# Kernel tuning notes

Hardware: AMD Instinct MI355X
Metric: run time of the kernel (lower is better)

The kernel has to match this reference:

```python
import jax, jax.numpy as jnp
import numpy as np

N = 50000      # nodes
E = 800000     # edges (avg degree 16)
IN, H, OUT = 512, 128, 64
L = 4          # num GCN layers
ALPHA = 0.1


def setup_inputs() -> dict:
    key = jax.random.key(0)
    ks = jax.random.split(key, 9)
    # GPRGNN layer weights: temp[k] = alpha*(1-alpha)^k, temp[L] = (1-alpha)^L
    temp = ALPHA * (1.0 - ALPHA) ** np.arange(L + 1)
    temp[-1] = (1.0 - ALPHA) ** L
    return {
        "x": jax.random.normal(ks[0], (N, IN), jnp.float32),
        "w": jax.random.uniform(ks[1], (E,), jnp.float32),
        "W_in": jax.random.normal(ks[2], (IN, H), jnp.float32) * (1.0 / np.sqrt(IN)),
        "b_in": jnp.zeros((H,), jnp.float32),
        "Wl": jax.random.normal(ks[3], (L, H, H), jnp.float32) * (1.0 / np.sqrt(H)),
        "bl": jnp.zeros((L, H), jnp.float32),
        "temp": jnp.asarray(temp, jnp.float32),
        "W_out": jax.random.normal(ks[4], (H, OUT), jnp.float32) * (1.0 / np.sqrt(H)),
        "b_out": jnp.zeros((OUT,), jnp.float32),
        "src": jax.random.randint(ks[5], (E,), 0, N, jnp.int32),
        "dst": jax.random.randint(ks[6], (E,), 0, N, jnp.int32),
    }


def reference(x, w, W_in, b_in, Wl, bl, temp, W_out, b_out, src, dst):
    # input linear projection
    h = x @ W_in + b_in                         # [N, H]
    hidden = temp[0] * h
    xcur = h
    for i in range(L):
        m = xcur @ Wl[i] + bl[i]                # per-layer GCN linear, [N, H]
        msg = w[:, None] * m[src]               # weighted gather, [E, H]
        agg = jax.ops.segment_sum(msg, dst, num_segments=N)  # scatter-sum, [N, H]
        xcur = jax.nn.relu(agg)                 # (dropout is eval-mode no-op)
        hidden = hidden + temp[i + 1] * xcur
    return hidden @ W_out + b_out               # [N, OUT]
```

## Files before the change

kernel.cpp:

```cpp
#include <hip/hip_runtime.h>


typedef __attribute__((ext_vector_type(8))) short short8;
typedef __attribute__((ext_vector_type(4))) float f32x4;

__device__ __forceinline__ unsigned short f2bf(float f) {
  union { float f; unsigned u; } c{f};
  unsigned u = c.u;
  return (unsigned short)((u + 0x7fff + ((u >> 16) & 1)) >> 16);
}
__device__ __forceinline__ float bf2f_lo(unsigned v) {
  return __uint_as_float(v << 16);
}
__device__ __forceinline__ float bf2f_hi(unsigned v) {
  return __uint_as_float(v & 0xffff0000u);
}
__device__ __forceinline__ unsigned pack2bf(float a, float b) {
  return (unsigned)f2bf(a) | ((unsigned)f2bf(b) << 16);
}

__device__ __forceinline__ void gll16(const void* g, void* l) {
  __builtin_amdgcn_global_load_lds(
      (const __attribute__((address_space(1))) unsigned int*)g,
      (__attribute__((address_space(3))) unsigned int*)l, 16, 0, 0);
}

__global__ void hist_kernel(const int* __restrict__ dst, int* __restrict__ deg, int E) {
  int e = blockIdx.x * blockDim.x + threadIdx.x;
  if (e < E) atomicAdd(&deg[dst[e]], 1);
}

__global__ __launch_bounds__(256) void scan_partial(const int* __restrict__ deg,
                                                    int* __restrict__ bsum, int N) {
  int b = blockIdx.x, t = threadIdx.x;
  int lane = t & 63, wave = t >> 6;
  int i0 = b * 1024 + t * 4;
  int s = 0;
  if (i0 + 3 < N) {
    int4 v = *(const int4*)&deg[i0];
    s = v.x + v.y + v.z + v.w;
  } else {
    for (int k = 0; k < 4; ++k)
      if (i0 + k < N) s += deg[i0 + k];
  }
  for (int d = 32; d; d >>= 1) s += __shfl_down(s, d, 64);
  __shared__ int ws[4];
  if (lane == 0) ws[wave] = s;
  __syncthreads();
  if (t == 0) bsum[b] = ws[0] + ws[1] + ws[2] + ws[3];
}

__global__ void scan_base(const int* __restrict__ bsum, int* __restrict__ base, int nb) {
  int l = threadIdx.x;
  int v = (l < nb) ? bsum[l] : 0;
  int incl = v;
  for (int d = 1; d < 64; d <<= 1) {
    int t = __shfl_up(incl, d, 64);
    if (l >= d) incl += t;
  }
  if (l < nb) base[l] = incl - v;
}

__global__ __launch_bounds__(256) void scan_emit(const int* __restrict__ deg,
                                                 const int* __restrict__ base,
                                                 int* __restrict__ rowptr,
                                                 int* __restrict__ cursor, int N, int E) {
  int b = blockIdx.x, t = threadIdx.x;
  int lane = t & 63, wave = t >> 6;
  int i0 = b * 1024 + t * 4;
  int d0 = 0, d1 = 0, d2 = 0, d3 = 0;
  if (i0 + 3 < N) {
    int4 v = *(const int4*)&deg[i0];
    d0 = v.x; d1 = v.y; d2 = v.z; d3 = v.w;
  } else {
    if (i0 < N) d0 = deg[i0];
    if (i0 + 1 < N) d1 = deg[i0 + 1];
    if (i0 + 2 < N) d2 = deg[i0 + 2];
    if (i0 + 3 < N) d3 = deg[i0 + 3];
  }
  int s = d0 + d1 + d2 + d3;
  int incl = s;
  for (int d = 1; d < 64; d <<= 1) {
    int tv = __shfl_up(incl, d, 64);
    if (lane >= d) incl += tv;
  }
  __shared__ int ws[4];
  if (lane == 63) ws[wave] = incl;
  __syncthreads();
  int woff = 0;
  for (int wv = 0; wv < wave; ++wv) woff += ws[wv];
  int off = base[b] + woff + incl - s;
  if (i0 < N)     { rowptr[i0] = off;                cursor[i0] = off; }
  if (i0 + 1 < N) { int o = off + d0;                rowptr[i0+1] = o; cursor[i0+1] = o; }
  if (i0 + 2 < N) { int o = off + d0 + d1;           rowptr[i0+2] = o; cursor[i0+2] = o; }
  if (i0 + 3 < N) { int o = off + d0 + d1 + d2;      rowptr[i0+3] = o; cursor[i0+3] = o; }
  if (b == 0 && t == 0) rowptr[N] = E;
}

__global__ void fill_kernel(const int* __restrict__ src, const int* __restrict__ dst,
                            const float* __restrict__ w, int* __restrict__ cursor,
                            int* __restrict__ esrc, float* __restrict__ ew, int E) {
  int e = blockIdx.x * blockDim.x + threadIdx.x;
  if (e < E) {
    int d = dst[e];
    int p = atomicAdd(&cursor[d], 1);
    esrc[p] = src[e];
    ew[p] = w[e];
  }
}

__global__ void conv_w_kernel(const float* __restrict__ W_in,
                              const float* __restrict__ Wl,
                              const float* __restrict__ W_out,
                              unsigned short* __restrict__ WinT,
                              unsigned short* __restrict__ WlT,
                              unsigned short* __restrict__ WoutT) {
  int o = blockIdx.x * blockDim.x + threadIdx.x;
  if (o < 65536) {
    int n = o >> 9, k = o & 511;
    WinT[o] = f2bf(W_in[k * 128 + n]);
  } else if (o < 131072) {
    int p = o - 65536;
    int layer = p >> 14, n = (p >> 7) & 127, k = p & 127;
    WlT[p] = f2bf(Wl[layer * 16384 + k * 128 + n]);
  } else if (o < 139264) {
    int p = o - 131072;
    int n = p >> 7, k = p & 127;
    WoutT[p] = f2bf(W_out[k * 64 + n]);
  }
}

template <int K, bool CONV>
__global__ __launch_bounds__(256) void gemm_bf16(
    const void* __restrict__ Ain, const unsigned short* __restrict__ BT,
    const float* __restrict__ bias, unsigned short* __restrict__ Cb, int M) {
  __shared__ unsigned short As[128 * 32];
  __shared__ unsigned short Bs[128 * 32];

  const int tid = threadIdx.x;
  const int lane = tid & 63;
  const int wave = tid >> 6;
  const int wm = (wave & 1) * 64;
  const int wn = (wave >> 1) * 64;
  const int blockRow = blockIdx.x * 128;

  f32x4 acc[4][4];
#pragma unroll
  for (int i = 0; i < 4; ++i)
#pragma unroll
    for (int j = 0; j < 4; ++j) acc[i][j] = (f32x4){0.f, 0.f, 0.f, 0.f};

  for (int k0 = 0; k0 < K; k0 += 32) {
    __syncthreads();
    if (CONV) {
      const float* A = (const float*)Ain;
      int row = tid >> 1;
      int kc = (tid & 1) * 16;
      int grow = blockRow + row;
      if (grow >= M) grow = M - 1;
      const float* s = &A[(size_t)grow * K + k0 + kc];
      float4 v0 = *(const float4*)(s);
      float4 v1 = *(const float4*)(s + 4);
      float4 v2 = *(const float4*)(s + 8);
      float4 v3 = *(const float4*)(s + 12);
      uint4 p0, p1;
      p0.x = pack2bf(v0.x, v0.y); p0.y = pack2bf(v0.z, v0.w);
      p0.z = pack2bf(v1.x, v1.y); p0.w = pack2bf(v1.z, v1.w);
      p1.x = pack2bf(v2.x, v2.y); p1.y = pack2bf(v2.z, v2.w);
      p1.z = pack2bf(v3.x, v3.y); p1.w = pack2bf(v3.z, v3.w);
      *(uint4*)&As[row * 32 + kc] = p0;
      *(uint4*)&As[row * 32 + kc + 8] = p1;
    } else {
      const unsigned short* A = (const unsigned short*)Ain;
#pragma unroll
      for (int ch = wave; ch < 8; ch += 4) {
        int row = ch * 16 + (lane >> 2);
        int grow = blockRow + row;
        if (grow >= M) grow = M - 1;
        gll16(&A[(size_t)grow * K + k0 + (lane & 3) * 8], (char*)As + ch * 1024);
      }
    }
#pragma unroll
    for (int ch = wave; ch < 8; ch += 4) {
      int row = ch * 16 + (lane >> 2);
      gll16(&BT[(size_t)row * K + k0 + (lane & 3) * 8], (char*)Bs + ch * 1024);
    }
    __syncthreads();

    short8 af[4], bfr[4];
#pragma unroll
    for (int i = 0; i < 4; ++i)
      af[i] = *(const short8*)&As[(wm + i * 16 + (lane & 15)) * 32 + (lane >> 4) * 8];
#pragma unroll
    for (int j = 0; j < 4; ++j)
      bfr[j] = *(const short8*)&Bs[(wn + j * 16 + (lane & 15)) * 32 + (lane >> 4) * 8];
#pragma unroll
    for (int i = 0; i < 4; ++i)
#pragma unroll
      for (int j = 0; j < 4; ++j)
        acc[i][j] =
            __builtin_amdgcn_mfma_f32_16x16x32_bf16(af[i], bfr[j], acc[i][j], 0, 0, 0);
  }

#pragma unroll
  for (int j = 0; j < 4; ++j) {
    int col = wn + j * 16 + (lane & 15);
    float bj = bias[col];
#pragma unroll
    for (int i = 0; i < 4; ++i) {
#pragma unroll
      for (int r = 0; r < 4; ++r) {
        int row = blockRow + wm + i * 16 + (lane >> 4) * 4 + r;
        if (row < M) Cb[(size_t)row * 128 + col] = f2bf(acc[i][j][r] + bj);
      }
    }
  }
}

__global__ __launch_bounds__(256) void agg_v3(
    const int* __restrict__ rowptr, const int* __restrict__ esrc,
    const float* __restrict__ ew, const unsigned short* __restrict__ mb,
    unsigned short* __restrict__ xnext, int N) {
  const int node = blockIdx.x * 4 + (threadIdx.x >> 6);
  const int lane = threadIdx.x & 63;
  if (node >= N) return;
  const int g = lane >> 4;
  const int c = lane & 15;
  const int beg = rowptr[node];
  const int end = rowptr[node + 1];
  const unsigned short* mc = mb + c * 8;

  float aA[8] = {0.f, 0.f, 0.f, 0.f, 0.f, 0.f, 0.f, 0.f};
  float aB[8] = {0.f, 0.f, 0.f, 0.f, 0.f, 0.f, 0.f, 0.f};

  int j = beg;
  for (; j + 8 <= end; j += 8) {
    int sA = esrc[j + g];     float wA = ew[j + g];
    int sB = esrc[j + 4 + g]; float wB = ew[j + 4 + g];
    uint4 vA = *(const uint4*)&mc[(size_t)sA * 128];
    uint4 vB = *(const uint4*)&mc[(size_t)sB * 128];
    aA[0] = fmaf(wA, bf2f_lo(vA.x), aA[0]); aA[1] = fmaf(wA, bf2f_hi(vA.x), aA[1]);
    aA[2] = fmaf(wA, bf2f_lo(vA.y), aA[2]); aA[3] = fmaf(wA, bf2f_hi(vA.y), aA[3]);
    aA[4] = fmaf(wA, bf2f_lo(vA.z), aA[4]); aA[5] = fmaf(wA, bf2f_hi(vA.z), aA[5]);
    aA[6] = fmaf(wA, bf2f_lo(vA.w), aA[6]); aA[7] = fmaf(wA, bf2f_hi(vA.w), aA[7]);
    aB[0] = fmaf(wB, bf2f_lo(vB.x), aB[0]); aB[1] = fmaf(wB, bf2f_hi(vB.x), aB[1]);
    aB[2] = fmaf(wB, bf2f_lo(vB.y), aB[2]); aB[3] = fmaf(wB, bf2f_hi(vB.y), aB[3]);
    aB[4] = fmaf(wB, bf2f_lo(vB.z), aB[4]); aB[5] = fmaf(wB, bf2f_hi(vB.z), aB[5]);
    aB[6] = fmaf(wB, bf2f_lo(vB.w), aB[6]); aB[7] = fmaf(wB, bf2f_hi(vB.w), aB[7]);
  }
  if (j + 4 <= end) {
    int s = esrc[j + g]; float wt = ew[j + g];
    uint4 v = *(const uint4*)&mc[(size_t)s * 128];
    aA[0] = fmaf(wt, bf2f_lo(v.x), aA[0]); aA[1] = fmaf(wt, bf2f_hi(v.x), aA[1]);
    aA[2] = fmaf(wt, bf2f_lo(v.y), aA[2]); aA[3] = fmaf(wt, bf2f_hi(v.y), aA[3]);
    aA[4] = fmaf(wt, bf2f_lo(v.z), aA[4]); aA[5] = fmaf(wt, bf2f_hi(v.z), aA[5]);
    aA[6] = fmaf(wt, bf2f_lo(v.w), aA[6]); aA[7] = fmaf(wt, bf2f_hi(v.w), aA[7]);
    j += 4;
  }
  if (j < end) {
    int idx = j + g;
    int s = esrc[(idx < end) ? idx : (end - 1)];
    float wt = (idx < end) ? ew[idx] : 0.f;
    uint4 v = *(const uint4*)&mc[(size_t)s * 128];
    aB[0] = fmaf(wt, bf2f_lo(v.x), aB[0]); aB[1] = fmaf(wt, bf2f_hi(v.x), aB[1]);
    aB[2] = fmaf(wt, bf2f_lo(v.y), aB[2]); aB[3] = fmaf(wt, bf2f_hi(v.y), aB[3]);
    aB[4] = fmaf(wt, bf2f_lo(v.z), aB[4]); aB[5] = fmaf(wt, bf2f_hi(v.z), aB[5]);
    aB[6] = fmaf(wt, bf2f_lo(v.w), aB[6]); aB[7] = fmaf(wt, bf2f_hi(v.w), aB[7]);
  }

  float r[8];
#pragma unroll
  for (int k = 0; k < 8; ++k) {
    float s = aA[k] + aB[k];
    s += __shfl_xor(s, 16, 64);
    s += __shfl_xor(s, 32, 64);
    r[k] = fmaxf(s, 0.f);
  }
  if (g == 0) {
    uint4 pk;
    pk.x = pack2bf(r[0], r[1]);
    pk.y = pack2bf(r[2], r[3]);
    pk.z = pack2bf(r[4], r[5]);
    pk.w = pack2bf(r[6], r[7]);
    *(uint4*)&xnext[(size_t)node * 128 + c * 8] = pk;
  }
}

__global__ __launch_bounds__(256) void gemm_out(
    const unsigned short* __restrict__ xb,
    const float* __restrict__ temp, const unsigned short* __restrict__ WoT,
    const float* __restrict__ b_out, float* __restrict__ out, int M) {
  __shared__ unsigned short As[128 * 136];
  __shared__ unsigned short Bs[64 * 136];

  const int tid = threadIdx.x;
  const int lane = tid & 63;
  const int wave = tid >> 6;
  const int blockRow = blockIdx.x * 128;

  float t[5];
#pragma unroll
  for (int i = 0; i < 5; ++i) t[i] = temp[i];

  {
    int row = tid >> 1;
    int grow = blockRow + row;
    if (grow >= M) grow = M - 1;
    int ch0 = (tid & 1) * 64;
#pragma unroll
    for (int gch = 0; gch < 64; gch += 8) {
      float acc[8] = {0.f, 0.f, 0.f, 0.f, 0.f, 0.f, 0.f, 0.f};
#pragma unroll
      for (int i = 0; i < 5; ++i) {
        uint4 v = *(const uint4*)&xb[((size_t)i * M + grow) * 128 + ch0 + gch];
        acc[0] = fmaf(t[i], bf2f_lo(v.x), acc[0]);
        acc[1] = fmaf(t[i], bf2f_hi(v.x), acc[1]);
        acc[2] = fmaf(t[i], bf2f_lo(v.y), acc[2]);
        acc[3] = fmaf(t[i], bf2f_hi(v.y), acc[3]);
        acc[4] = fmaf(t[i], bf2f_lo(v.z), acc[4]);
        acc[5] = fmaf(t[i], bf2f_hi(v.z), acc[5]);
        acc[6] = fmaf(t[i], bf2f_lo(v.w), acc[6]);
        acc[7] = fmaf(t[i], bf2f_hi(v.w), acc[7]);
      }
      uint4 pk;
      pk.x = pack2bf(acc[0], acc[1]);
      pk.y = pack2bf(acc[2], acc[3]);
      pk.z = pack2bf(acc[4], acc[5]);
      pk.w = pack2bf(acc[6], acc[7]);
      *(uint4*)&As[row * 136 + ch0 + gch] = pk;
    }
  }
  for (int i = tid; i < 64 * 16; i += 256) {
    int row = i >> 4;
    int chunk = (i & 15) * 8;
    *(uint4*)&Bs[row * 136 + chunk] = *(const uint4*)&WoT[row * 128 + chunk];
  }
  __syncthreads();

  f32x4 acc[2][4];
#pragma unroll
  for (int i = 0; i < 2; ++i)
#pragma unroll
    for (int j = 0; j < 4; ++j) acc[i][j] = (f32x4){0.f, 0.f, 0.f, 0.f};

#pragma unroll
  for (int kf = 0; kf < 4; ++kf) {
    short8 af[2], bfr[4];
#pragma unroll
    for (int i = 0; i < 2; ++i)
      af[i] = *(const short8*)&As[(wave * 32 + i * 16 + (lane & 15)) * 136 + kf * 32 +
                                  (lane >> 4) * 8];
#pragma unroll
    for (int j = 0; j < 4; ++j)
      bfr[j] = *(const short8*)&Bs[(j * 16 + (lane & 15)) * 136 + kf * 32 +
                                   (lane >> 4) * 8];
#pragma unroll
    for (int i = 0; i < 2; ++i)
#pragma unroll
      for (int j = 0; j < 4; ++j)
        acc[i][j] =
            __builtin_amdgcn_mfma_f32_16x16x32_bf16(af[i], bfr[j], acc[i][j], 0, 0, 0);
  }

#pragma unroll
  for (int j = 0; j < 4; ++j) {
    int col = j * 16 + (lane & 15);
    float bj = b_out[col];
#pragma unroll
    for (int i = 0; i < 2; ++i) {
#pragma unroll
      for (int r = 0; r < 4; ++r) {
        int row = blockRow + wave * 32 + i * 16 + (lane >> 4) * 4 + r;
        if (row < M) out[(size_t)row * 64 + col] = acc[i][j][r] + bj;
      }
    }
  }
}

extern "C" void kernel_launch(void* const* d_in, const int* in_sizes, int n_in,
                              void* d_out, int out_size, void* d_ws, size_t ws_size,
                              hipStream_t stream) {
  const float* x     = (const float*)d_in[0];
  const float* w     = (const float*)d_in[1];
  const float* W_in  = (const float*)d_in[2];
  const float* b_in  = (const float*)d_in[3];
  const float* Wl    = (const float*)d_in[4];
  const float* bl    = (const float*)d_in[5];
  const float* temp  = (const float*)d_in[6];
  const float* W_out = (const float*)d_in[7];
  const float* b_out = (const float*)d_in[8];
  const int*   src   = (const int*)d_in[9];
  const int*   dst   = (const int*)d_in[10];

  const int IN = 512, H = 128, L = 4;
  const int N = in_sizes[0] / IN;
  const int E = in_sizes[1];
  const int NB = (N + 1023) / 1024;
  const size_t NH = (size_t)N * H;

  char* p = (char*)d_ws;
  auto alloc = [&](size_t bytes) {
    void* r = (void*)p;
    p += (bytes + 255) & ~(size_t)255;
    return r;
  };
  unsigned short* xb     = (unsigned short*)alloc(5 * NH * 2);
  unsigned short* mbuf_b = (unsigned short*)alloc(NH * 2);
  unsigned short* WinT   = (unsigned short*)alloc((size_t)H * IN * 2);
  unsigned short* WlT    = (unsigned short*)alloc((size_t)L * H * H * 2);
  unsigned short* WoutT  = (unsigned short*)alloc((size_t)64 * H * 2);
  int*   deg    = (int*)alloc((size_t)N * sizeof(int));
  int*   rowptr = (int*)alloc((size_t)(N + 1) * sizeof(int));
  int*   cursor = (int*)alloc((size_t)N * sizeof(int));
  int*   esrc   = (int*)alloc((size_t)E * sizeof(int));
  float* ew     = (float*)alloc((size_t)E * sizeof(float));
  int*   bsum   = (int*)alloc(64 * sizeof(int));
  int*   base   = (int*)alloc(64 * sizeof(int));

  hipMemsetAsync(deg, 0, (size_t)N * sizeof(int), stream);
  hist_kernel<<<(E + 255) / 256, 256, 0, stream>>>(dst, deg, E);
  scan_partial<<<NB, 256, 0, stream>>>(deg, bsum, N);
  scan_base<<<1, 64, 0, stream>>>(bsum, base, NB);
  scan_emit<<<NB, 256, 0, stream>>>(deg, base, rowptr, cursor, N, E);
  fill_kernel<<<(E + 255) / 256, 256, 0, stream>>>(src, dst, w, cursor, esrc, ew, E);
  conv_w_kernel<<<544, 256, 0, stream>>>(W_in, Wl, W_out, WinT, WlT, WoutT);

  const int gB = (N + 127) / 128;

  gemm_bf16<512, true><<<gB, 256, 0, stream>>>(x, WinT, b_in, xb, N);

  for (int i = 0; i < L; ++i) {
    gemm_bf16<128, false><<<gB, 256, 0, stream>>>(
        xb + (size_t)i * NH, WlT + (size_t)i * H * H, bl + (size_t)i * H, mbuf_b, N);
    agg_v3<<<(N + 3) / 4, 256, 0, stream>>>(rowptr, esrc, ew, mbuf_b,
                                            xb + (size_t)(i + 1) * NH, N);
  }

  gemm_out<<<gB, 256, 0, stream>>>(xb, temp, WoutT, b_out, (float*)d_out, N);
}
```

Before: 506.7 us.

## Aggregate before the linear transform and fuse gather with per-layer GEMM

Uses linearity to compute (A·x)·W + (Σw)·b in place of A·(x·W + b). Each block gathers neighbours for 128 nodes into LDS as bf16, then runs the 128x128 MFMA GEMM on that tile, adding the weight-sum-scaled bias and ReLU. This removes the intermediate message buffer round trip and one launch per layer. In exchange, the gather now runs with far fewer waves, each handling 32 nodes serially, so latency hiding drops. It also adds a bf16 rounding of the aggregate before the GEMM.

```diff
diff --git a/kernel.cpp b/kernel.cpp
--- a/kernel.cpp
+++ b/kernel.cpp
@@ -217,72 +217,142 @@
   }
 }
 
-__global__ __launch_bounds__(256) void agg_v3(
+__global__ __launch_bounds__(256) void layer_fused(
     const int* __restrict__ rowptr, const int* __restrict__ esrc,
-    const float* __restrict__ ew, const unsigned short* __restrict__ mb,
-    unsigned short* __restrict__ xnext, int N) {
-  const int node = blockIdx.x * 4 + (threadIdx.x >> 6);
-  const int lane = threadIdx.x & 63;
-  if (node >= N) return;
+    const float* __restrict__ ew, const unsigned short* __restrict__ xin,
+    const unsigned short* __restrict__ WlTl, const float* __restrict__ bl,
+    unsigned short* __restrict__ xout, int N) {
+  __shared__ unsigned short As[128 * 136];
+  __shared__ float wsumS[128];
+  __shared__ unsigned short Bs[128 * 32];
+
+  const int tid = threadIdx.x;
+  const int lane = tid & 63;
+  const int wave = tid >> 6;
   const int g = lane >> 4;
   const int c = lane & 15;
-  const int beg = rowptr[node];
-  const int end = rowptr[node + 1];
-  const unsigned short* mc = mb + c * 8;
-
-  float aA[8] = {0.f, 0.f, 0.f, 0.f, 0.f, 0.f, 0.f, 0.f};
-  float aB[8] = {0.f, 0.f, 0.f, 0.f, 0.f, 0.f, 0.f, 0.f};
-
-  int j = beg;
-  for (; j + 8 <= end; j += 8) {
-    int sA = esrc[j + g];     float wA = ew[j + g];
-    int sB = esrc[j + 4 + g]; float wB = ew[j + 4 + g];
-    uint4 vA = *(const uint4*)&mc[(size_t)sA * 128];
-    uint4 vB = *(const uint4*)&mc[(size_t)sB * 128];
-    aA[0] = fmaf(wA, bf2f_lo(vA.x), aA[0]); aA[1] = fmaf(wA, bf2f_hi(vA.x), aA[1]);
-    aA[2] = fmaf(wA, bf2f_lo(vA.y), aA[2]); aA[3] = fmaf(wA, bf2f_hi(vA.y), aA[3]);
-    aA[4] = fmaf(wA, bf2f_lo(vA.z), aA[4]); aA[5] = fmaf(wA, bf2f_hi(vA.z), aA[5]);
-    aA[6] = fmaf(wA, bf2f_lo(vA.w), aA[6]); aA[7] = fmaf(wA, bf2f_hi(vA.w), aA[7]);
-    aB[0] = fmaf(wB, bf2f_lo(vB.x), aB[0]); aB[1] = fmaf(wB, bf2f_hi(vB.x), aB[1]);
-    aB[2] = fmaf(wB, bf2f_lo(vB.y), aB[2]); aB[3] = fmaf(wB, bf2f_hi(vB.y), aB[3]);
-    aB[4] = fmaf(wB, bf2f_lo(vB.z), aB[4]); aB[5] = fmaf(wB, bf2f_hi(vB.z), aB[5]);
-    aB[6] = fmaf(wB, bf2f_lo(vB.w), aB[6]); aB[7] = fmaf(wB, bf2f_hi(vB.w), aB[7]);
-  }
-  if (j + 4 <= end) {
-    int s = esrc[j + g]; float wt = ew[j + g];
-    uint4 v = *(const uint4*)&mc[(size_t)s * 128];
-    aA[0] = fmaf(wt, bf2f_lo(v.x), aA[0]); aA[1] = fmaf(wt, bf2f_hi(v.x), aA[1]);
-    aA[2] = fmaf(wt, bf2f_lo(v.y), aA[2]); aA[3] = fmaf(wt, bf2f_hi(v.y), aA[3]);
-    aA[4] = fmaf(wt, bf2f_lo(v.z), aA[4]); aA[5] = fmaf(wt, bf2f_hi(v.z), aA[5]);
-    aA[6] = fmaf(wt, bf2f_lo(v.w), aA[6]); aA[7] = fmaf(wt, bf2f_hi(v.w), aA[7]);
-    j += 4;
-  }
-  if (j < end) {
-    int idx = j + g;
-    int s = esrc[(idx < end) ? idx : (end - 1)];
-    float wt = (idx < end) ? ew[idx] : 0.f;
-    uint4 v = *(const uint4*)&mc[(size_t)s * 128];
-    aB[0] = fmaf(wt, bf2f_lo(v.x), aB[0]); aB[1] = fmaf(wt, bf2f_hi(v.x), aB[1]);
-    aB[2] = fmaf(wt, bf2f_lo(v.y), aB[2]); aB[3] = fmaf(wt, bf2f_hi(v.y), aB[3]);
-    aB[4] = fmaf(wt, bf2f_lo(v.z), aB[4]); aB[5] = fmaf(wt, bf2f_hi(v.z), aB[5]);
-    aB[6] = fmaf(wt, bf2f_lo(v.w), aB[6]); aB[7] = fmaf(wt, bf2f_hi(v.w), aB[7]);
-  }
-
-  float r[8];
-#pragma unroll
-  for (int k = 0; k < 8; ++k) {
-    float s = aA[k] + aB[k];
-    s += __shfl_xor(s, 16, 64);
-    s += __shfl_xor(s, 32, 64);
-    r[k] = fmaxf(s, 0.f);
-  }
-  if (g == 0) {
-    uint4 pk;
-    pk.x = pack2bf(r[0], r[1]);
-    pk.y = pack2bf(r[2], r[3]);
-    pk.z = pack2bf(r[4], r[5]);
-    pk.w = pack2bf(r[6], r[7]);
-    *(uint4*)&xnext[(size_t)node * 128 + c * 8] = pk;
+  const int blockRow = blockIdx.x * 128;
+  const unsigned short* mc = xin + c * 8;
+
+  for (int t = 0; t < 32; ++t) {
+    const int nl = wave * 32 + t;
+    const int node = blockRow + nl;
+    float aA[8] = {0.f, 0.f, 0.f, 0.f, 0.f, 0.f, 0.f, 0.f};
+    float aB[8] = {0.f, 0.f, 0.f, 0.f, 0.f, 0.f, 0.f, 0.f};
+    float wsA = 0.f, wsB = 0.f;
+    if (node < N) {
+      const int beg = rowptr[node];
+      const int end = rowptr[node + 1];
+      int j = beg;
+      for (; j + 8 <= end; j += 8) {
+        int sA = esrc[j + g];     float wA = ew[j + g];
+        int sB = esrc[j + 4 + g]; float wB = ew[j + 4 + g];
+        uint4 vA = *(const uint4*)&mc[(size_t)sA * 128];
+        uint4 vB = *(const uint4*)&mc[(size_t)sB * 128];
+        wsA += wA; wsB += wB;
+        aA[0] = fmaf(wA, bf2f_lo(vA.x), aA[0]); aA[1] = fmaf(wA, bf2f_hi(vA.x), aA[1]);
+        aA[2] = fmaf(wA, bf2f_lo(vA.y), aA[2]); aA[3] = fmaf(wA, bf2f_hi(vA.y), aA[3]);
+        aA[4] = fmaf(wA, bf2f_lo(vA.z), aA[4]); aA[5] = fmaf(wA, bf2f_hi(vA.z), aA[5]);
+        aA[6] = fmaf(wA, bf2f_lo(vA.w), aA[6]); aA[7] = fmaf(wA, bf2f_hi(vA.w), aA[7]);
+        aB[0] = fmaf(wB, bf2f_lo(vB.x), aB[0]); aB[1] = fmaf(wB, bf2f_hi(vB.x), aB[1]);
+        aB[2] = fmaf(wB, bf2f_lo(vB.y), aB[2]); aB[3] = fmaf(wB, bf2f_hi(vB.y), aB[3]);
+        aB[4] = fmaf(wB, bf2f_lo(vB.z), aB[4]); aB[5] = fmaf(wB, bf2f_hi(vB.z), aB[5]);
+        aB[6] = fmaf(wB, bf2f_lo(vB.w), aB[6]); aB[7] = fmaf(wB, bf2f_hi(vB.w), aB[7]);
+      }
+      if (j + 4 <= end) {
+        int s = esrc[j + g]; float wt = ew[j + g];
+        uint4 v = *(const uint4*)&mc[(size_t)s * 128];
+        wsA += wt;
+        aA[0] = fmaf(wt, bf2f_lo(v.x), aA[0]); aA[1] = fmaf(wt, bf2f_hi(v.x), aA[1]);
+        aA[2] = fmaf(wt, bf2f_lo(v.y), aA[2]); aA[3] = fmaf(wt, bf2f_hi(v.y), aA[3]);
+        aA[4] = fmaf(wt, bf2f_lo(v.z), aA[4]); aA[5] = fmaf(wt, bf2f_hi(v.z), aA[5]);
+        aA[6] = fmaf(wt, bf2f_lo(v.w), aA[6]); aA[7] = fmaf(wt, bf2f_hi(v.w), aA[7]);
+        j += 4;
+      }
+      if (j < end) {
+        int idx = j + g;
+        int s = esrc[(idx < end) ? idx : (end - 1)];
+        float wt = (idx < end) ? ew[idx] : 0.f;
+        uint4 v = *(const uint4*)&mc[(size_t)s * 128];
+        wsB += wt;
+        aB[0] = fmaf(wt, bf2f_lo(v.x), aB[0]); aB[1] = fmaf(wt, bf2f_hi(v.x), aB[1]);
+        aB[2] = fmaf(wt, bf2f_lo(v.y), aB[2]); aB[3] = fmaf(wt, bf2f_hi(v.y), aB[3]);
+        aB[4] = fmaf(wt, bf2f_lo(v.z), aB[4]); aB[5] = fmaf(wt, bf2f_hi(v.z), aB[5]);
+        aB[6] = fmaf(wt, bf2f_lo(v.w), aB[6]); aB[7] = fmaf(wt, bf2f_hi(v.w), aB[7]);
+      }
+    }
+    float ws = wsA + wsB;
+    ws += __shfl_xor(ws, 16, 64);
+    ws += __shfl_xor(ws, 32, 64);
+    float r[8];
+#pragma unroll
+    for (int k = 0; k < 8; ++k) {
+      float s = aA[k] + aB[k];
+      s += __shfl_xor(s, 16, 64);
+      s += __shfl_xor(s, 32, 64);
+      r[k] = s;
+    }
+    if (g == 0) {
+      uint4 pk;
+      pk.x = pack2bf(r[0], r[1]);
+      pk.y = pack2bf(r[2], r[3]);
+      pk.z = pack2bf(r[4], r[5]);
+      pk.w = pack2bf(r[6], r[7]);
+      *(uint4*)&As[nl * 136 + c * 8] = pk;
+      if (c == 0) wsumS[nl] = ws;
+    }
+  }
+  __syncthreads();
+
+  const int wm = (wave & 1) * 64;
+  const int wn = (wave >> 1) * 64;
+  f32x4 acc[4][4];
+#pragma unroll
+  for (int i = 0; i < 4; ++i)
+#pragma unroll
+    for (int j = 0; j < 4; ++j) acc[i][j] = (f32x4){0.f, 0.f, 0.f, 0.f};
+
+  for (int k0 = 0; k0 < 128; k0 += 32) {
+    if (k0) __syncthreads();
+#pragma unroll
+    for (int ch = wave; ch < 8; ch += 4) {
+      int row = ch * 16 + (lane >> 2);
+      gll16(&WlTl[(size_t)row * 128 + k0 + (lane & 3) * 8], (char*)Bs + ch * 1024);
+    }
+    __syncthreads();
+
+    short8 af[4], bfr[4];
+#pragma unroll
+    for (int i = 0; i < 4; ++i)
+      af[i] = *(const short8*)&As[(wm + i * 16 + (lane & 15)) * 136 + k0 +
+                                  (lane >> 4) * 8];
+#pragma unroll
+    for (int j = 0; j < 4; ++j)
+      bfr[j] = *(const short8*)&Bs[(wn + j * 16 + (lane & 15)) * 32 + (lane >> 4) * 8];
+#pragma unroll
+    for (int i = 0; i < 4; ++i)
+#pragma unroll
+      for (int j = 0; j < 4; ++j)
+        acc[i][j] =
+            __builtin_amdgcn_mfma_f32_16x16x32_bf16(af[i], bfr[j], acc[i][j], 0, 0, 0);
+  }
+
+#pragma unroll
+  for (int j = 0; j < 4; ++j) {
+    int col = wn + j * 16 + (lane & 15);
+    float blv = bl[col];
+#pragma unroll
+    for (int i = 0; i < 4; ++i) {
+#pragma unroll
+      for (int r = 0; r < 4; ++r) {
+        int rl = wm + i * 16 + (lane >> 4) * 4 + r;
+        int row = blockRow + rl;
+        if (row < N) {
+          float v = fmaxf(fmaf(wsumS[rl], blv, acc[i][j][r]), 0.f);
+          xout[(size_t)row * 128 + col] = f2bf(v);
+        }
+      }
+    }
   }
 }
 
@@ -405,7 +475,6 @@
     return r;
   };
   unsigned short* xb     = (unsigned short*)alloc(5 * NH * 2);
-  unsigned short* mbuf_b = (unsigned short*)alloc(NH * 2);
   unsigned short* WinT   = (unsigned short*)alloc((size_t)H * IN * 2);
   unsigned short* WlT    = (unsigned short*)alloc((size_t)L * H * H * 2);
   unsigned short* WoutT  = (unsigned short*)alloc((size_t)64 * H * 2);
@@ -430,10 +499,9 @@
   gemm_bf16<512, true><<<gB, 256, 0, stream>>>(x, WinT, b_in, xb, N);
 
   for (int i = 0; i < L; ++i) {
-    gemm_bf16<128, false><<<gB, 256, 0, stream>>>(
-        xb + (size_t)i * NH, WlT + (size_t)i * H * H, bl + (size_t)i * H, mbuf_b, N);
-    agg_v3<<<(N + 3) / 4, 256, 0, stream>>>(rowptr, esrc, ew, mbuf_b,
-                                            xb + (size_t)(i + 1) * NH, N);
+    layer_fused<<<gB, 256, 0, stream>>>(rowptr, esrc, ew, xb + (size_t)i * NH,
+                                        WlT + (size_t)i * H * H, bl + (size_t)i * H,
+                                        xb + (size_t)(i + 1) * NH, N);
   }
 
   gemm_out<<<gB, 256, 0, stream>>>(xb, temp, WoutT, b_out, (float*)d_out, N);
```

Measured after the change: 694.9 us. +37.1%, slower.
